# Kernel optimization log

Measured on AMD Instinct MI355X. Metric: run time of the kernel, lower is better.

## Reference

```python
import jax, jax.numpy as jnp
import numpy as np

B, N, S, C, H = 8, 1024, 16, 3, 8   # batch, num_patches, spatial side, num_channels, heads
DIM = S * S * C                      # 768 = per-token feature size = dim
HD = DIM // H                        # head dim actually used = 96
SCALE = float(HD) ** -0.5            # dim//num_heads == p//num_heads here
REATTEN_SCALE = 1.0                  # transform_scale=False
BN_EPS = 1e-3                        # Keras BatchNormalization default epsilon


def _conv3x3(x, w):
    # x: [B*N, S, S, C], w: [3, 3, Cin, Cout], SAME padding, no bias (qkv_bias=False)
    return jax.lax.conv_general_dilated(
        x, w, window_strides=(1, 1), padding='SAME',
        dimension_numbers=('NHWC', 'HWIO', 'NHWC'))


def _make_heads(x5):
    # x5: [B, N, S, S, C] -> [B, H, N, HD]
    x = x5.reshape(B, N, DIM).reshape(B, N, H, HD)
    return x.transpose(0, 2, 1, 3)


def setup_inputs():
    key = jax.random.key(0)
    ks = jax.random.split(key, 14)
    f = lambda k, sh, s=1.0: jax.random.normal(k, sh, jnp.float32) * s
    return {
        'q': f(ks[0], (B, N, DIM)),
        'k': f(ks[1], (B, N, DIM)),
        'v': f(ks[2], (B, N, DIM)),
        'wq': f(ks[3], (3, 3, C, C), 0.2),
        'wk': f(ks[4], (3, 3, C, C), 0.2),
        'wv': f(ks[5], (3, 3, C, C), 0.2),
        'w_re': f(ks[6], (N, N), 0.03),          # 1x1 conv kernel [in=N, out=N]
        'b_re': f(ks[7], (N,), 0.02),
        'bn_gamma': 1.0 + f(ks[8], (N,), 0.05),
        'bn_beta': f(ks[9], (N,), 0.05),
        'bn_mean': f(ks[10], (N,), 0.05),
        'bn_var': jax.random.uniform(ks[11], (N,), jnp.float32, 0.5, 1.5),
        'w_proj': f(ks[12], (DIM, DIM), 0.03),
        'b_proj': f(ks[13], (DIM,), 0.02),
    }


def reference(q, k, v, wq, wk, wv, w_re, b_re, bn_gamma, bn_beta, bn_mean, bn_var,
              w_proj, b_proj):
    def qkv(x, w):
        # unflatten [B,N,p] -> [B*N,S,S,C], 3x3 conv (map_fn over batch == batched conv)
        xi = x.reshape(B * N, S, S, C)
        return _make_heads(_conv3x3(xi, w).reshape(B, N, S, S, C))

    qh, kh, vh = qkv(q, wq), qkv(k, wk), qkv(v, wv)        # [B,H,N,HD]
    attn = jnp.einsum('bhnd,bhmd->bhnm', qh, kh) * SCALE    # [B,H,N,N]
    attn = jax.nn.softmax(attn, axis=-1)
    # re-attention: 1x1 conv over channel (last) axis + inference BatchNorm
    attn = jnp.einsum('bhnm,mp->bhnp', attn, w_re) + b_re
    attn = (attn - bn_mean) * jax.lax.rsqrt(bn_var + BN_EPS) * bn_gamma + bn_beta
    attn = attn * REATTEN_SCALE
    x = jnp.einsum('bhnm,bhmd->bhnd', attn, vh)             # [B,H,N,HD]
    x = x.transpose(0, 2, 1, 3).reshape(B, N, DIM)
    return x @ w_proj + b_proj
```

## Files before the change

### kernel.cpp

```cpp
#include <hip/hip_runtime.h>
#include <hip/hip_bf16.h>


typedef __attribute__((ext_vector_type(4))) float f32x4;
typedef __bf16 __attribute__((ext_vector_type(8))) bf16x8;
typedef unsigned short u16x8 __attribute__((ext_vector_type(8)));

__device__ __forceinline__ unsigned short f2bf(float x){
  unsigned u = __builtin_bit_cast(unsigned, x);
  u += 0x7fffu + ((u >> 16) & 1u);
  return (unsigned short)(u >> 16);
}

__device__ __forceinline__ float bf2f(unsigned short u){
  unsigned v = (unsigned)u << 16;
  return __builtin_bit_cast(float, v);
}

__device__ __forceinline__ f32x4 mfma16(bf16x8 a, bf16x8 b, f32x4 c){
  return __builtin_amdgcn_mfma_f32_16x16x32_bf16(a, b, c, 0, 0, 0);
}

__device__ __forceinline__ bf16x8 ld8(const unsigned short* p){
  return *reinterpret_cast<const bf16x8*>(p);
}

__global__ void prep_kernel(const float* __restrict__ w_re, const float* __restrict__ b_re,
                            const float* __restrict__ gma, const float* __restrict__ beta,
                            const float* __restrict__ mean, const float* __restrict__ var,
                            unsigned short* __restrict__ Wre_rm,
                            float* __restrict__ G, float* __restrict__ Cc,
                            float* __restrict__ CoverG)
{
  int idx = blockIdx.x * 256 + threadIdx.x;
  if (idx < 1024*1024){
    Wre_rm[idx] = f2bf(w_re[idx]);
  } else if (idx < 1024*1024 + 1024){
    int p = idx - 1024*1024;
    float g = gma[p] * rsqrtf(var[p] + 1e-3f);
    float cc = (b_re[p] - mean[p]) * g + beta[p];
    G[p] = g;
    Cc[p] = cc;
    CoverG[p] = cc / g;
  }
}

__global__ __launch_bounds__(256) void wpt_kernel(const float* __restrict__ wp,
                                                  unsigned short* __restrict__ Wpt)
{
  __shared__ float t[64][65];
  const int i0 = blockIdx.x * 64, o0 = blockIdx.y * 64;
  const int r = threadIdx.x >> 6;
  const int c = threadIdx.x & 63;
#pragma unroll
  for (int rep = 0; rep < 16; ++rep){
    int row = rep*4 + r;
    t[row][c] = wp[(size_t)(i0 + row)*768 + o0 + c];
  }
  __syncthreads();
#pragma unroll
  for (int rep = 0; rep < 16; ++rep){
    int orow = rep*4 + r;
    Wpt[(size_t)(o0 + orow)*768 + i0 + c] = f2bf(t[c][orow]);
  }
}

__global__ __launch_bounds__(256, 4) void conv_kernel(
    const float* __restrict__ q, const float* __restrict__ k,
    const float* __restrict__ v,
    const float* __restrict__ wq, const float* __restrict__ wk,
    const float* __restrict__ wv,
    const float* __restrict__ G,
    unsigned short* __restrict__ qh, unsigned short* __restrict__ kh,
    unsigned short* __restrict__ vh)
{
  const int tb = blockIdx.x;
  const int which = blockIdx.y;
  const float* x = (which == 0) ? q : (which == 1) ? k : v;
  const float* w = (which == 0) ? wq : (which == 1) ? wk : wv;
  unsigned short* dst = (which == 0) ? qh : (which == 1) ? kh : vh;

  float wreg[81];
#pragma unroll
  for (int i = 0; i < 81; ++i) wreg[i] = w[i];

  const int tid = threadIdx.x;
  const int c = tid & 15, r = tid >> 4;

  float msk[9];
  int   off[9];
#pragma unroll
  for (int dr = 0; dr < 3; ++dr)
#pragma unroll
    for (int dc = 0; dc < 3; ++dc){
      int rr = r + dr - 1, cc = c + dc - 1;
      bool valid = (rr >= 0) && (rr < 16) && (cc >= 0) && (cc < 16);
      int rc = rr < 0 ? 0 : (rr > 15 ? 15 : rr);
      int cl = cc < 0 ? 0 : (cc > 15 ? 15 : cc);
      msk[dr*3 + dc] = valid ? 1.f : 0.f;
      off[dr*3 + dc] = (rc*16 + cl)*3;
    }

#pragma unroll
  for (int tk = 0; tk < 4; ++tk){
    const float* xt = x + ((size_t)(tb*4 + tk))*768;
    float a0 = 0.f, a1 = 0.f, a2 = 0.f;
#pragma unroll
    for (int j = 0; j < 9; ++j){
      const float* p = xt + off[j];
      float m = msk[j];
      float x0 = p[0]*m, x1 = p[1]*m, x2 = p[2]*m;
      const int wb = j*9;
      a0 += x0*wreg[wb+0] + x1*wreg[wb+3] + x2*wreg[wb+6];
      a1 += x0*wreg[wb+1] + x1*wreg[wb+4] + x2*wreg[wb+7];
      a2 += x0*wreg[wb+2] + x1*wreg[wb+5] + x2*wreg[wb+8];
    }
    const int token = tb*4 + tk;
    const int b = token >> 10, n = token & 1023;
    const float gs = (which == 2) ? G[n] : 1.f;
    float av[3] = {a0*gs, a1*gs, a2*gs};
#pragma unroll
    for (int co = 0; co < 3; ++co){
      int f = tid*3 + co;
      int h = f / 96, d = f - h*96;
      dst[((size_t)(b*8 + h)*1024 + n)*96 + d] = f2bf(av[co]);
    }
  }
}

__global__ __launch_bounds__(256) void vt_kernel(const unsigned short* __restrict__ vh,
                                                 const float* __restrict__ CoverG,
                                                 unsigned short* __restrict__ vtg,
                                                 float* __restrict__ cvpart)
{
  __shared__ unsigned short t[96*136];
  const int chunk = blockIdx.x;
  const int bh = blockIdx.y;
  const int n0 = chunk*128;
  const int tid = threadIdx.x;

  const unsigned short* src = vh + ((size_t)bh*1024 + n0)*96;
#pragma unroll
  for (int it = 0; it < 6; ++it){
    int idx = it*256 + tid;
    int row = idx / 12, v = idx - row*12;
    u16x8 xv = *reinterpret_cast<const u16x8*>(src + row*96 + v*8);
#pragma unroll
    for (int j = 0; j < 8; ++j) t[(v*8 + j)*136 + row] = xv[j];
  }
  __syncthreads();

  unsigned short* dstp = vtg + (size_t)bh*96*1024 + n0;
#pragma unroll
  for (int it = 0; it < 6; ++it){
    int idx = it*256 + tid;
    int d = idx >> 4, ch = idx & 15;
    u16x8 xv = *reinterpret_cast<const u16x8*>(&t[d*136 + ch*8]);
    *reinterpret_cast<u16x8*>(dstp + (size_t)d*1024 + ch*8) = xv;

    float s = 0.f;
#pragma unroll
    for (int j = 0; j < 8; ++j) s += CoverG[n0 + ch*8 + j] * bf2f(xv[j]);
#pragma unroll
    for (int o = 1; o < 16; o <<= 1) s += __shfl_xor(s, o);
    if (ch == 0) cvpart[((size_t)chunk*64 + bh)*96 + d] = s;
  }
}

__global__ __launch_bounds__(256, 2) void m2_kernel(
    const unsigned short* __restrict__ Wre_rm, const unsigned short* __restrict__ vtg,
    unsigned short* __restrict__ M2t)
{
  constexpr int WST = 40;
  constexpr int VST = 40;
  __shared__ __align__(16) unsigned short Wst[2][128*WST];
  __shared__ __align__(16) unsigned short Vst[2][96*VST];

  const int id = blockIdx.x;
  const int xcd = id & 7, slot = id >> 3;
  const int mtile = slot & 7;
  const int bh = xcd + ((slot >> 3) << 3);
  const int tid = threadIdx.x;
  const int w = tid >> 6, lane = tid & 63, lh = lane >> 4, lm = lane & 15;
  const int m0 = mtile*128;
  const int mw = w*32;

  const unsigned short* vb = vtg + (size_t)bh * 96 * 1024;
  const unsigned short* Wb = Wre_rm + (size_t)m0 * 1024;

  const int cr = tid >> 2, cc0 = (tid & 3)*8;
  const bool has3 = (tid < 128);

  f32x4 acc[2][6];
#pragma unroll
  for (int rt = 0; rt < 2; ++rt)
#pragma unroll
    for (int dt = 0; dt < 6; ++dt)
      acc[rt][dt] = f32x4{0.f, 0.f, 0.f, 0.f};

  u16x8 g0, g1, g2, g3;
  g0 = *reinterpret_cast<const u16x8*>(Wb + (size_t)cr*1024 + cc0);
  g1 = *reinterpret_cast<const u16x8*>(Wb + (size_t)(64 + cr)*1024 + cc0);
  g2 = *reinterpret_cast<const u16x8*>(vb + (size_t)cr*1024 + cc0);
  if (has3) g3 = *reinterpret_cast<const u16x8*>(vb + (size_t)(64 + cr)*1024 + cc0);
  *reinterpret_cast<u16x8*>(&Wst[0][cr*WST + cc0]) = g0;
  *reinterpret_cast<u16x8*>(&Wst[0][(64 + cr)*WST + cc0]) = g1;
  *reinterpret_cast<u16x8*>(&Vst[0][cr*VST + cc0]) = g2;
  if (has3) *reinterpret_cast<u16x8*>(&Vst[0][(64 + cr)*VST + cc0]) = g3;
  __syncthreads();

  for (int ks = 0; ks < 32; ++ks){
    const int cur = ks & 1;

    if (ks < 31){
      const int p0 = (ks+1)*32;
      g0 = *reinterpret_cast<const u16x8*>(Wb + (size_t)cr*1024 + p0 + cc0);
      g1 = *reinterpret_cast<const u16x8*>(Wb + (size_t)(64 + cr)*1024 + p0 + cc0);
      g2 = *reinterpret_cast<const u16x8*>(vb + (size_t)cr*1024 + p0 + cc0);
      if (has3) g3 = *reinterpret_cast<const u16x8*>(vb + (size_t)(64 + cr)*1024 + p0 + cc0);
    }

    const unsigned short* Wc = &Wst[cur][0];
    const unsigned short* Vc = &Vst[cur][0];
    bf16x8 aW0 = ld8(Wc + (mw + lm)*WST + lh*8);
    bf16x8 aW1 = ld8(Wc + (mw + 16 + lm)*WST + lh*8);
#pragma unroll
    for (int dt = 0; dt < 6; ++dt){
      bf16x8 bV = ld8(Vc + (dt*16 + lm)*VST + lh*8);
      acc[0][dt] = mfma16(aW0, bV, acc[0][dt]);
      acc[1][dt] = mfma16(aW1, bV, acc[1][dt]);
    }

    if (ks < 31){
      const int nxt = cur ^ 1;
      *reinterpret_cast<u16x8*>(&Wst[nxt][cr*WST + cc0]) = g0;
      *reinterpret_cast<u16x8*>(&Wst[nxt][(64 + cr)*WST + cc0]) = g1;
      *reinterpret_cast<u16x8*>(&Vst[nxt][cr*VST + cc0]) = g2;
      if (has3) *reinterpret_cast<u16x8*>(&Vst[nxt][(64 + cr)*VST + cc0]) = g3;
    }
    __syncthreads();
  }

#pragma unroll
  for (int rt = 0; rt < 2; ++rt)
#pragma unroll
    for (int dt = 0; dt < 6; ++dt)
#pragma unroll
      for (int rg = 0; rg < 4; ++rg){
        int m = m0 + mw + rt*16 + lh*4 + rg;
        int d = dt*16 + lm;
        M2t[((size_t)bh*96 + d)*1024 + m] = f2bf(acc[rt][dt][rg]);
      }
}

__global__ __launch_bounds__(256, 2) void attn_kernel(
    const unsigned short* __restrict__ qh, const unsigned short* __restrict__ kh,
    const unsigned short* __restrict__ M2t, const float* __restrict__ cvpart,
    unsigned short* __restrict__ xh)
{
  constexpr int KST = 104;
  constexpr int MST = 40;
  constexpr int PST = 40;
  __shared__ __align__(16) unsigned short Kst[2][32*KST];
  __shared__ __align__(16) unsigned short Mst[2][96*MST];
  __shared__ __align__(16) unsigned short Pst[2][4][32*PST];

  const int id = blockIdx.x;
  const int xcd = id & 7, slot = id >> 3;
  const int chunk = slot & 7;
  const int bh = xcd + ((slot >> 3) << 3);
  const int tid = threadIdx.x;
  const int w = tid >> 6;
  const int lane = tid & 63;
  const int lh = lane >> 4;
  const int lm = lane & 15;
  const int q0 = chunk*128 + w*32;

  const unsigned short* Qb = qh + (size_t)bh * 1024 * 96;
  const unsigned short* Kb = kh + (size_t)bh * 1024 * 96;
  const unsigned short* Mb = M2t + (size_t)bh * 96 * 1024;

  const int kr0 = tid/12,  kc0 = (tid%12)*8;
  const bool c1K = (tid < 128);
  const int t1 = tid + 256;
  const int kr1 = c1K ? t1/12 : 0,  kc1 = c1K ? (t1%12)*8 : 0;
  const int md1 = c1K ? 0 : (tid-128)>>2, mc1 = c1K ? 0 : ((tid-128)&3)*8;
  const int md2 = (tid+128)>>2, mc2 = ((tid+128)&3)*8;

  bf16x8 aq[2][3];
#pragma unroll
  for (int rt = 0; rt < 2; ++rt)
#pragma unroll
    for (int kq = 0; kq < 3; ++kq)
      aq[rt][kq] = ld8(Qb + (size_t)(q0 + rt*16 + lm)*96 + kq*32 + lh*8);

  f32x4 out[2][6];
#pragma unroll
  for (int rt = 0; rt < 2; ++rt)
#pragma unroll
    for (int dt = 0; dt < 6; ++dt) out[rt][dt] = f32x4{0.f, 0.f, 0.f, 0.f};
  f32x4 ssum[2] = {f32x4{0.f,0.f,0.f,0.f}, f32x4{0.f,0.f,0.f,0.f}};

  const float SCALE = 0.10206207261596577f;

  u16x8 g0, g1, g2;
  {
    g0 = *reinterpret_cast<const u16x8*>(Kb + (size_t)kr0*96 + kc0);
    g1 = c1K ? *reinterpret_cast<const u16x8*>(Kb + (size_t)kr1*96 + kc1)
             : *reinterpret_cast<const u16x8*>(Mb + (size_t)md1*1024 + mc1);
    g2 = *reinterpret_cast<const u16x8*>(Mb + (size_t)md2*1024 + mc2);
    *reinterpret_cast<u16x8*>(&Kst[0][kr0*KST + kc0]) = g0;
    if (c1K) *reinterpret_cast<u16x8*>(&Kst[0][kr1*KST + kc1]) = g1;
    else     *reinterpret_cast<u16x8*>(&Mst[0][md1*MST + mc1]) = g1;
    *reinterpret_cast<u16x8*>(&Mst[0][md2*MST + mc2]) = g2;
  }
  __syncthreads();

  for (int kt = 0; kt < 32; ++kt){
    const int cur = kt & 1;

    if (kt < 31){
      const int kb = (kt+1)*32;
      g0 = *reinterpret_cast<const u16x8*>(Kb + (size_t)(kb + kr0)*96 + kc0);
      g1 = c1K ? *reinterpret_cast<const u16x8*>(Kb + (size_t)(kb + kr1)*96 + kc1)
               : *reinterpret_cast<const u16x8*>(Mb + (size_t)md1*1024 + kb + mc1);
      g2 = *reinterpret_cast<const u16x8*>(Mb + (size_t)md2*1024 + kb + mc2);
    }

    const unsigned short* Kc = &Kst[cur][0];
    f32x4 sacc[2][2];
    sacc[0][0] = f32x4{0.f,0.f,0.f,0.f}; sacc[0][1] = f32x4{0.f,0.f,0.f,0.f};
    sacc[1][0] = f32x4{0.f,0.f,0.f,0.f}; sacc[1][1] = f32x4{0.f,0.f,0.f,0.f};
#pragma unroll
    for (int kq = 0; kq < 3; ++kq){
      bf16x8 bk0 = ld8(Kc + lm*KST        + kq*32 + lh*8);
      bf16x8 bk1 = ld8(Kc + (16 + lm)*KST + kq*32 + lh*8);
      sacc[0][0] = mfma16(aq[0][kq], bk0, sacc[0][0]);
      sacc[0][1] = mfma16(aq[0][kq], bk1, sacc[0][1]);
      sacc[1][0] = mfma16(aq[1][kq], bk0, sacc[1][0]);
      sacc[1][1] = mfma16(aq[1][kq], bk1, sacc[1][1]);
    }

    unsigned short* Pc = &Pst[cur][w][0];
#pragma unroll
    for (int rt = 0; rt < 2; ++rt)
#pragma unroll
      for (int nt = 0; nt < 2; ++nt)
#pragma unroll
        for (int rg = 0; rg < 4; ++rg){
          float e = __expf(sacc[rt][nt][rg] * SCALE);
          ssum[rt][rg] += e;
          Pc[(rt*16 + lh*4 + rg)*PST + nt*16 + lm] = f2bf(e);
        }

    bf16x8 ap0 = ld8(Pc + lm*PST        + lh*8);
    bf16x8 ap1 = ld8(Pc + (16 + lm)*PST + lh*8);

    const unsigned short* Mc = &Mst[cur][0];
#pragma unroll
    for (int dt = 0; dt < 6; ++dt){
      bf16x8 bm = ld8(Mc + (dt*16 + lm)*MST + lh*8);
      out[0][dt] = mfma16(ap0, bm, out[0][dt]);
      out[1][dt] = mfma16(ap1, bm, out[1][dt]);
    }

    if (kt < 31){
      const int nxt = cur ^ 1;
      *reinterpret_cast<u16x8*>(&Kst[nxt][kr0*KST + kc0]) = g0;
      if (c1K) *reinterpret_cast<u16x8*>(&Kst[nxt][kr1*KST + kc1]) = g1;
      else     *reinterpret_cast<u16x8*>(&Mst[nxt][md1*MST + mc1]) = g1;
      *reinterpret_cast<u16x8*>(&Mst[nxt][md2*MST + mc2]) = g2;
    }
    __syncthreads();
  }

#pragma unroll
  for (int rt = 0; rt < 2; ++rt)
#pragma unroll
    for (int rg = 0; rg < 4; ++rg){
      float s = ssum[rt][rg];
#pragma unroll
      for (int off = 1; off < 16; off <<= 1) s += __shfl_xor(s, off);
      ssum[rt][rg] = 1.f / s;
    }

#pragma unroll
  for (int dt = 0; dt < 6; ++dt){
    float cvv = 0.f;
#pragma unroll
    for (int ch = 0; ch < 8; ++ch)
      cvv += cvpart[((size_t)ch*64 + bh)*96 + dt*16 + lm];
#pragma unroll
    for (int rt = 0; rt < 2; ++rt)
#pragma unroll
      for (int rg = 0; rg < 4; ++rg){
        int row = q0 + rt*16 + lh*4 + rg;
        xh[((size_t)bh*1024 + row)*96 + dt*16 + lm] =
            f2bf(out[rt][dt][rg]*ssum[rt][rg] + cvv);
      }
  }
}

__global__ __launch_bounds__(256, 2) void proj_kernel(
    const unsigned short* __restrict__ xh, const unsigned short* __restrict__ Wpt,
    const float* __restrict__ b_proj, float* __restrict__ out)
{
  constexpr int BST = 40;
  __shared__ __align__(16) unsigned short Bst[2][96*BST];

  const int mb = blockIdx.x;
  const int nb = blockIdx.y;
  const int tid = threadIdx.x;
  const int w = tid >> 6, lane = tid & 63, lh = lane >> 4, lm = lane & 15;
  const int t0 = mb*128 + w*32;
  const int o0 = nb*96;

  const int br0 = tid >> 2,          bc0 = (tid & 3)*8;
  const bool has1 = (tid < 128);
  const int br1 = (tid + 256) >> 2,  bc1 = ((tid + 256) & 3)*8;
  const unsigned short* Bsrc = Wpt + (size_t)o0*768;

  f32x4 acc[2][6];
#pragma unroll
  for (int rt = 0; rt < 2; ++rt)
#pragma unroll
    for (int nt = 0; nt < 6; ++nt) acc[rt][nt] = f32x4{0.f, 0.f, 0.f, 0.f};

  const int tok0 = t0 + lm, tok1 = t0 + 16 + lm;
  const int b0 = tok0 >> 10, n0_ = tok0 & 1023;
  const int b1 = tok1 >> 10, n1_ = tok1 & 1023;

  u16x8 g0, g1;
  g0 = *reinterpret_cast<const u16x8*>(Bsrc + (size_t)br0*768 + bc0);
  if (has1) g1 = *reinterpret_cast<const u16x8*>(Bsrc + (size_t)br1*768 + bc1);
  *reinterpret_cast<u16x8*>(&Bst[0][br0*BST + bc0]) = g0;
  if (has1) *reinterpret_cast<u16x8*>(&Bst[0][br1*BST + bc1]) = g1;
  __syncthreads();

  for (int kt = 0; kt < 24; ++kt){
    const int cur = kt & 1;

    if (kt < 23){
      const int ib = (kt+1)*32;
      g0 = *reinterpret_cast<const u16x8*>(Bsrc + (size_t)br0*768 + ib + bc0);
      if (has1) g1 = *reinterpret_cast<const u16x8*>(Bsrc + (size_t)br1*768 + ib + bc1);
    }

    const int h = kt/3, d0 = (kt - h*3)*32 + lh*8;
    bf16x8 a0 = ld8(xh + ((size_t)(b0*8 + h)*1024 + n0_)*96 + d0);
    bf16x8 a1 = ld8(xh + ((size_t)(b1*8 + h)*1024 + n1_)*96 + d0);

    const unsigned short* Bc = &Bst[cur][0];
#pragma unroll
    for (int nt = 0; nt < 6; ++nt){
      bf16x8 bv = ld8(Bc + (nt*16 + lm)*BST + lh*8);
      acc[0][nt] = mfma16(a0, bv, acc[0][nt]);
      acc[1][nt] = mfma16(a1, bv, acc[1][nt]);
    }

    if (kt < 23){
      const int nxt = cur ^ 1;
      *reinterpret_cast<u16x8*>(&Bst[nxt][br0*BST + bc0]) = g0;
      if (has1) *reinterpret_cast<u16x8*>(&Bst[nxt][br1*BST + bc1]) = g1;
    }
    __syncthreads();
  }

#pragma unroll
  for (int nt = 0; nt < 6; ++nt){
    int o = o0 + nt*16 + lm;
    float bias = b_proj[o];
#pragma unroll
    for (int rt = 0; rt < 2; ++rt)
#pragma unroll
      for (int rg = 0; rg < 4; ++rg)
        out[(size_t)(t0 + rt*16 + lh*4 + rg)*768 + o] = acc[rt][nt][rg] + bias;
  }
}

extern "C" void kernel_launch(void* const* d_in, const int* in_sizes, int n_in,
                              void* d_out, int out_size, void* d_ws, size_t ws_size,
                              hipStream_t stream)
{
  (void)in_sizes; (void)n_in; (void)out_size; (void)ws_size;
  const float* q      = (const float*)d_in[0];
  const float* k      = (const float*)d_in[1];
  const float* v      = (const float*)d_in[2];
  const float* wq     = (const float*)d_in[3];
  const float* wk     = (const float*)d_in[4];
  const float* wv     = (const float*)d_in[5];
  const float* w_re   = (const float*)d_in[6];
  const float* b_re   = (const float*)d_in[7];
  const float* gma    = (const float*)d_in[8];
  const float* beta   = (const float*)d_in[9];
  const float* mean   = (const float*)d_in[10];
  const float* var    = (const float*)d_in[11];
  const float* w_proj = (const float*)d_in[12];
  const float* b_proj = (const float*)d_in[13];
  float* out = (float*)d_out;

  char* ws = (char*)d_ws;
  unsigned short* qh     = (unsigned short*)(ws + 0);
  unsigned short* kh     = (unsigned short*)(ws + 12582912);
  unsigned short* vtg    = (unsigned short*)(ws + 25165824);
  unsigned short* xh     = (unsigned short*)(ws + 37748736);
  unsigned short* vh     = xh;
  unsigned short* Wre_rm = (unsigned short*)(ws + 50331648);
  unsigned short* Wpt    = (unsigned short*)(ws + 52428800);
  unsigned short* M2t    = (unsigned short*)(ws + 53608448);
  float*          G      = (float*)(ws + 66191360);
  float*          Cc     = (float*)(ws + 66195456);
  float*          CoverG = (float*)(ws + 66199552);
  float*          cvpart = (float*)(ws + 66203648);

  prep_kernel<<<dim3(4100), dim3(256), 0, stream>>>(w_re, b_re, gma, beta, mean, var,
                                                    Wre_rm, G, Cc, CoverG);
  wpt_kernel<<<dim3(12, 12), dim3(256), 0, stream>>>(w_proj, Wpt);
  conv_kernel<<<dim3(2048, 3), dim3(256), 0, stream>>>(q, k, v, wq, wk, wv, G, qh, kh, vh);
  vt_kernel<<<dim3(8, 64), dim3(256), 0, stream>>>(vh, CoverG, vtg, cvpart);
  m2_kernel<<<dim3(512), dim3(256), 0, stream>>>(Wre_rm, vtg, M2t);
  attn_kernel<<<dim3(512), dim3(256), 0, stream>>>(qh, kh, M2t, cvpart, xh);
  proj_kernel<<<dim3(64, 8), dim3(256), 0, stream>>>(xh, Wpt, b_proj, out);
}
```

Baseline: 143.8 us.

## Restructure conv kernel: one image row per thread with vectorized loads and stores

The 3x3 conv kernel now gives each thread a whole 16-pixel image row of one token, 16 tokens per block. It loads the three neighbouring rows with 16-byte vector loads into registers and writes 48 packed bf16 outputs with 16-byte stores. Before, each thread computed one pixel and did scalar gathers plus 2-byte scattered stores. This cuts memory transactions and redundant loads, at the cost of many more registers (launch bounds lowered to 2 blocks) and fewer blocks in the grid.

```diff
diff --git a/kernel.cpp b/kernel.cpp
--- a/kernel.cpp
+++ b/kernel.cpp
@@ -5,6 +5,7 @@
 typedef __attribute__((ext_vector_type(4))) float f32x4;
 typedef __bf16 __attribute__((ext_vector_type(8))) bf16x8;
 typedef unsigned short u16x8 __attribute__((ext_vector_type(8)));
+typedef unsigned int u32x4 __attribute__((ext_vector_type(4)));
 
 __device__ __forceinline__ unsigned short f2bf(float x){
   unsigned u = __builtin_bit_cast(unsigned, x);
@@ -65,7 +66,7 @@
   }
 }
 
-__global__ __launch_bounds__(256, 4) void conv_kernel(
+__global__ __launch_bounds__(256, 2) void conv_kernel(
     const float* __restrict__ q, const float* __restrict__ k,
     const float* __restrict__ v,
     const float* __restrict__ wq, const float* __restrict__ wk,
@@ -85,46 +86,74 @@
   for (int i = 0; i < 81; ++i) wreg[i] = w[i];
 
   const int tid = threadIdx.x;
-  const int c = tid & 15, r = tid >> 4;
-
-  float msk[9];
-  int   off[9];
-#pragma unroll
-  for (int dr = 0; dr < 3; ++dr)
+  const int ti = tid >> 4;
+  const int r  = tid & 15;
+  const int token = tb*16 + ti;
+  const float* xt = x + (size_t)token*768;
+
+  const int rm = (r > 0)  ? r-1 : 0;
+  const int rp = (r < 15) ? r+1 : 15;
+  const float mm = (r > 0)  ? 1.f : 0.f;
+  const float mp = (r < 15) ? 1.f : 0.f;
+
+  f32x4 Rm[12], R0[12], Rp[12];
+#pragma unroll
+  for (int j = 0; j < 12; ++j){
+    Rm[j] = *reinterpret_cast<const f32x4*>(xt + rm*48 + j*4);
+    R0[j] = *reinterpret_cast<const f32x4*>(xt + r *48 + j*4);
+    Rp[j] = *reinterpret_cast<const f32x4*>(xt + rp*48 + j*4);
+  }
+#pragma unroll
+  for (int j = 0; j < 12; ++j){
+    Rm[j] = Rm[j] * mm;
+    Rp[j] = Rp[j] * mp;
+  }
+
+  const float gs = (which == 2) ? G[token & 1023] : 1.f;
+
+  unsigned int pk[24];
+
+#pragma unroll
+  for (int c = 0; c < 16; ++c){
+    float a0 = 0.f, a1 = 0.f, a2 = 0.f;
 #pragma unroll
     for (int dc = 0; dc < 3; ++dc){
-      int rr = r + dr - 1, cc = c + dc - 1;
-      bool valid = (rr >= 0) && (rr < 16) && (cc >= 0) && (cc < 16);
-      int rc = rr < 0 ? 0 : (rr > 15 ? 15 : rr);
-      int cl = cc < 0 ? 0 : (cc > 15 ? 15 : cc);
-      msk[dr*3 + dc] = valid ? 1.f : 0.f;
-      off[dr*3 + dc] = (rc*16 + cl)*3;
-    }
-
-#pragma unroll
-  for (int tk = 0; tk < 4; ++tk){
-    const float* xt = x + ((size_t)(tb*4 + tk))*768;
-    float a0 = 0.f, a1 = 0.f, a2 = 0.f;
-#pragma unroll
-    for (int j = 0; j < 9; ++j){
-      const float* p = xt + off[j];
-      float m = msk[j];
-      float x0 = p[0]*m, x1 = p[1]*m, x2 = p[2]*m;
-      const int wb = j*9;
-      a0 += x0*wreg[wb+0] + x1*wreg[wb+3] + x2*wreg[wb+6];
-      a1 += x0*wreg[wb+1] + x1*wreg[wb+4] + x2*wreg[wb+7];
-      a2 += x0*wreg[wb+2] + x1*wreg[wb+5] + x2*wreg[wb+8];
-    }
-    const int token = tb*4 + tk;
-    const int b = token >> 10, n = token & 1023;
-    const float gs = (which == 2) ? G[n] : 1.f;
-    float av[3] = {a0*gs, a1*gs, a2*gs};
-#pragma unroll
-    for (int co = 0; co < 3; ++co){
-      int f = tid*3 + co;
-      int h = f / 96, d = f - h*96;
-      dst[((size_t)(b*8 + h)*1024 + n)*96 + d] = f2bf(av[co]);
-    }
+      const int cc = c + dc - 1;
+      if (cc < 0 || cc > 15) continue;
+#pragma unroll
+      for (int ci = 0; ci < 3; ++ci){
+        const int e = cc*3 + ci;
+        const float xm = Rm[e >> 2][e & 3];
+        const float x0 = R0[e >> 2][e & 3];
+        const float xp = Rp[e >> 2][e & 3];
+        const int w0 = (0*3 + dc)*9 + ci*3;
+        const int w1 = (1*3 + dc)*9 + ci*3;
+        const int w2 = (2*3 + dc)*9 + ci*3;
+        a0 += xm*wreg[w0+0] + x0*wreg[w1+0] + xp*wreg[w2+0];
+        a1 += xm*wreg[w0+1] + x0*wreg[w1+1] + xp*wreg[w2+1];
+        a2 += xm*wreg[w0+2] + x0*wreg[w1+2] + xp*wreg[w2+2];
+      }
+    }
+    const unsigned short b0 = f2bf(a0*gs), b1 = f2bf(a1*gs), b2 = f2bf(a2*gs);
+    const int f = c*3;
+    if ((f & 1) == 0){
+      pk[f>>1] = (unsigned)b0 | ((unsigned)b1 << 16);
+      pk[(f+2)>>1] = (unsigned)b2;
+    } else {
+      pk[f>>1] |= ((unsigned)b0 << 16);
+      pk[(f+1)>>1] = (unsigned)b1 | ((unsigned)b2 << 16);
+    }
+  }
+
+  const int b = token >> 10, n = token & 1023;
+  const int h = r >> 1;
+  unsigned short* dstp = dst + ((size_t)(b*8 + h)*1024 + n)*96 + (r & 1)*48;
+#pragma unroll
+  for (int j = 0; j < 6; ++j){
+    u32x4 sv;
+#pragma unroll
+    for (int e = 0; e < 4; ++e) sv[e] = pk[j*4 + e];
+    *reinterpret_cast<u32x4*>(dstp + j*8) = sv;
   }
 }
 
@@ -516,7 +545,7 @@
   prep_kernel<<<dim3(4100), dim3(256), 0, stream>>>(w_re, b_re, gma, beta, mean, var,
                                                     Wre_rm, G, Cc, CoverG);
   wpt_kernel<<<dim3(12, 12), dim3(256), 0, stream>>>(w_proj, Wpt);
-  conv_kernel<<<dim3(2048, 3), dim3(256), 0, stream>>>(q, k, v, wq, wk, wv, G, qh, kh, vh);
+  conv_kernel<<<dim3(512, 3), dim3(256), 0, stream>>>(q, k, v, wq, wk, wv, G, qh, kh, vh);
   vt_kernel<<<dim3(8, 64), dim3(256), 0, stream>>>(vh, CoverG, vtg, cvpart);
   m2_kernel<<<dim3(512), dim3(256), 0, stream>>>(Wre_rm, vtg, M2t);
   attn_kernel<<<dim3(512), dim3(256), 0, stream>>>(qh, kh, M2t, cvpart, xh);
```

Measured after the change: 145.6 us. Within noise of the previous version (+1.2%).
